# Performance work log

Measured on AMD Instinct MI355X. Metric: run time of the kernel, lower is better.

Reference implementation:

```python
import jax, jax.numpy as jnp
import numpy as np

B, L, H, S = 64, 1024, 768, 32
NH, HD = 8, H // 8
SEP = 102
EPS_LN = 1e-5


def setup_inputs() -> dict:
    key = jax.random.key(0)
    ks = jax.random.split(key, 16)
    # input_ids with exactly S SEP tokens per row at positions (j+1)*(L//S)-1
    ids = jax.random.randint(ks[0], (B, L), 1000, 30000, dtype=jnp.int64)
    sep_idx = (jnp.arange(1, S + 1) * (L // S)) - 1  # [S]
    ids = ids.at[:, sep_idx].set(SEP)
    attention_mask = jnp.ones((B, L), dtype=jnp.int32)
    labels = jax.random.randint(ks[1], (B, S), 0, 2, dtype=jnp.int64)
    sequence_output = jax.random.normal(ks[2], (B, L, H), dtype=jnp.float32)
    sc = 0.02
    params = dict(
        enc_W=jax.random.normal(ks[3], (H, H), jnp.float32) * sc,
        enc_b=jnp.zeros((H,), jnp.float32),
        enc_ln_g=jnp.ones((H,), jnp.float32),
        enc_ln_b=jnp.zeros((H,), jnp.float32),
        in_proj_W=jax.random.normal(ks[4], (3 * H, H), jnp.float32) * sc,
        in_proj_b=jnp.zeros((3 * H,), jnp.float32),
        out_proj_W=jax.random.normal(ks[5], (H, H), jnp.float32) * sc,
        out_proj_b=jnp.zeros((H,), jnp.float32),
        cls_W1=jax.random.normal(ks[6], (H, H), jnp.float32) * sc,
        cls_b1=jnp.zeros((H,), jnp.float32),
        cls_ln_g=jnp.ones((H,), jnp.float32),
        cls_ln_b=jnp.zeros((H,), jnp.float32),
        cls_W2=jax.random.normal(ks[7], (2, H), jnp.float32) * sc,
        cls_b2=jnp.zeros((2,), jnp.float32),
    )
    return dict(input_ids=ids, attention_mask=attention_mask, labels=labels,
                sequence_output=sequence_output, **params)


def _layernorm(x, g, b):
    m = jnp.mean(x, axis=-1, keepdims=True)
    v = jnp.mean((x - m) ** 2, axis=-1, keepdims=True)
    return (x - m) * jax.lax.rsqrt(v + EPS_LN) * g + b


def _gelu(x):
    return jax.nn.gelu(x, approximate=False)


def reference(input_ids, attention_mask, labels, sequence_output,
              enc_W, enc_b, enc_ln_g, enc_ln_b,
              in_proj_W, in_proj_b, out_proj_W, out_proj_b,
              cls_W1, cls_b1, cls_ln_g, cls_ln_b, cls_W2, cls_b2):
    # sep positions per sample (exactly S per row by construction)
    sep_pos = jax.vmap(lambda r: jnp.nonzero(r == SEP, size=S, fill_value=L - 1)[0])(input_ids)  # [B,S]
    all_pos = jnp.concatenate([jnp.zeros((B, 1), sep_pos.dtype), sep_pos], axis=1)  # [B,S+1]
    starts, ends = all_pos[:, :S], all_pos[:, 1:]  # inclusive [start, end] as in slice start:end+1
    t = jnp.arange(L)
    seg = (t[None, None, :] >= starts[:, :, None]) & (t[None, None, :] <= ends[:, :, None])  # [B,S,L]
    m = seg.astype(jnp.float32) * attention_mask[:, None, :].astype(jnp.float32)
    denom = jnp.sum(m, axis=-1, keepdims=True) + 1e-10  # [B,S,1]
    reps = jnp.einsum('bsl,bld->bsd', m, sequence_output) / denom  # segment mean pool
    # sentence encoder: Linear -> LN -> (dropout off) -> GELU
    x = _gelu(_layernorm(reps @ enc_W.T + enc_b, enc_ln_g, enc_ln_b))  # [B,S,H]
    # per-sample MHA (self-attention over sentences), dropout off
    qkv = x @ in_proj_W.T + in_proj_b  # [B,S,3H]
    q, k, v = jnp.split(qkv, 3, axis=-1)
    def heads(z):
        return z.reshape(B, S, NH, HD).transpose(0, 2, 1, 3)  # [B,NH,S,HD]
    q, k, v = heads(q), heads(k), heads(v)
    scores = jnp.einsum('bhqd,bhkd->bhqk', q, k) / jnp.sqrt(jnp.float32(HD))
    attn = jax.nn.softmax(scores, axis=-1)
    o = jnp.einsum('bhqk,bhkd->bhqd', attn, v).transpose(0, 2, 1, 3).reshape(B, S, H)
    attended = o @ out_proj_W.T + out_proj_b
    # classifier
    h = _gelu(_layernorm(attended @ cls_W1.T + cls_b1, cls_ln_g, cls_ln_b))
    logits = h @ cls_W2.T + cls_b2  # [B,S,2] (current_sentences == max_sentences, no padding)
    # cross entropy with ignore_index=-100
    flat_logits = logits.reshape(-1, 2)
    flat_labels = labels.reshape(-1)
    valid = flat_labels != -100
    safe = jnp.where(valid, flat_labels, 0)
    logp = jax.nn.log_softmax(flat_logits, axis=-1)
    nll = -jnp.take_along_axis(logp, safe[:, None], axis=-1)[:, 0]
    loss = jnp.sum(jnp.where(valid, nll, 0.0)) / jnp.maximum(jnp.sum(valid), 1)
    return loss, logits
```

## Files before the change

kernel.cpp:

```cpp
#include <hip/hip_runtime.h>
#include <math.h>

#define Bdim 64
#define Ldim 1024
#define Hdim 768
#define Sdim 32
#define NHdim 8
#define HDdim 96
#define SEP_ID 102

typedef unsigned short ushort_t;
typedef __attribute__((ext_vector_type(8))) short bf16x8;
typedef __attribute__((ext_vector_type(4))) float f32x4;

__device__ __forceinline__ ushort_t f2b(float f) {
    unsigned u = __builtin_bit_cast(unsigned, f);
    u += 0x7fffu + ((u >> 16) & 1u);
    return (ushort_t)(u >> 16);
}
__device__ __forceinline__ float b2f(ushort_t v) {
    unsigned u = ((unsigned)v) << 16;
    return __builtin_bit_cast(float, u);
}

__global__ __launch_bounds__(192) void prep_pool_kernel(const float* __restrict__ seq,
                                                        const int* __restrict__ ids,
                                                        const int* __restrict__ amask,
                                                        const float* __restrict__ w0,
                                                        const float* __restrict__ w1,
                                                        const float* __restrict__ w2,
                                                        const float* __restrict__ w3,
                                                        ushort_t* __restrict__ wdst,
                                                        ushort_t* __restrict__ reps) {
    int blk = blockIdx.x;
    int t = threadIdx.x;
    if (blk >= 2048) {
        int idx = (blk - 2048) * 192 + t;
        const float* src; int off;
        if (idx < 147456)      { src = w0; off = idx; }
        else if (idx < 589824) { src = w1; off = idx - 147456; }
        else if (idx < 737280) { src = w2; off = idx - 589824; }
        else                   { src = w3; off = idx - 737280; }
        float4 v = ((const float4*)src)[off];
        ushort4 ov; ov.x = f2b(v.x); ov.y = f2b(v.y); ov.z = f2b(v.z); ov.w = f2b(v.w);
        ((ushort4*)wdst)[idx] = ov;
        return;
    }
    int b = blk >> 5, s = blk & 31;
    __shared__ unsigned long long masks[18];
    const int* idrow = ids + (size_t)b * Ldim;
    int wv = t >> 6, ln = t & 63;
#pragma unroll
    for (int r = 0; r < 6; ++r) {
        int p = r * 192 + t;
        bool is = (p < Ldim) && (idrow[p] == SEP_ID);
        unsigned long long m = __ballot(is);
        if (ln == 0) masks[r * 3 + wv] = m;
    }
    __syncthreads();
    int start, end;
    {
        int need0 = s - 1, need1 = s;
        int p0 = Ldim - 1, p1 = Ldim - 1;
        int cnt = 0;
#pragma unroll
        for (int i = 0; i < 18; ++i) {
            unsigned long long mk = masks[i];
            int pc = __popcll(mk);
            int base = (i / 3) * 192 + (i % 3) * 64;
            if (need0 >= cnt && need0 < cnt + pc) {
                unsigned long long mm = mk;
                for (int j = cnt; j < need0; ++j) mm &= mm - 1;
                p0 = base + __ffsll(mm) - 1;
            }
            if (need1 >= cnt && need1 < cnt + pc) {
                unsigned long long mm = mk;
                for (int j = cnt; j < need1; ++j) mm &= mm - 1;
                p1 = base + __ffsll(mm) - 1;
            }
            cnt += pc;
        }
        start = (s == 0) ? 0 : p0;
        end = p1;
    }
    const float* base = seq + (size_t)b * Ldim * Hdim;
    const int* am = amask + b * Ldim;
    float4 A0 = {0,0,0,0}, A1 = {0,0,0,0};
    float d0 = 0.f, d1 = 0.f;
    int l = start;
    for (; l + 7 <= end; l += 8) {
        float m[8]; float4 v[8];
#pragma unroll
        for (int r = 0; r < 8; ++r) m[r] = (float)am[l + r];
#pragma unroll
        for (int r = 0; r < 8; ++r) v[r] = ((const float4*)(base + (size_t)(l + r) * Hdim))[t];
#pragma unroll
        for (int r = 0; r < 8; ++r) {
            if (r & 1) {
                d1 += m[r];
                A1.x += m[r] * v[r].x; A1.y += m[r] * v[r].y;
                A1.z += m[r] * v[r].z; A1.w += m[r] * v[r].w;
            } else {
                d0 += m[r];
                A0.x += m[r] * v[r].x; A0.y += m[r] * v[r].y;
                A0.z += m[r] * v[r].z; A0.w += m[r] * v[r].w;
            }
        }
    }
    for (; l <= end; ++l) {
        float m0 = (float)am[l];
        float4 v0 = ((const float4*)(base + (size_t)l * Hdim))[t];
        d0 += m0;
        A0.x += m0 * v0.x; A0.y += m0 * v0.y; A0.z += m0 * v0.z; A0.w += m0 * v0.w;
    }
    float denom = d0 + d1;
    float inv = 1.f / (denom + 1e-10f);
    float4 acc;
    acc.x = (A0.x + A1.x) * inv;
    acc.y = (A0.y + A1.y) * inv;
    acc.z = (A0.z + A1.z) * inv;
    acc.w = (A0.w + A1.w) * inv;
    ushort4 o;
    o.x = f2b(acc.x); o.y = f2b(acc.y); o.z = f2b(acc.z); o.w = f2b(acc.w);
    ((ushort4*)(reps + (size_t)blk * Hdim))[t] = o;
}

__global__ __launch_bounds__(256) void gemm_mfma(const ushort_t* __restrict__ A,
                                                 const ushort_t* __restrict__ W,
                                                 const float* __restrict__ bias,
                                                 ushort_t* __restrict__ Cout,
                                                 int M, int N, int K) {
    __shared__ __attribute__((aligned(16))) ushort_t Al[2][64][64];
    __shared__ __attribute__((aligned(16))) ushort_t Bl[2][64][64];
    int tid = threadIdx.x;
    int wid = tid >> 6, lane = tid & 63;
    int rowBase = blockIdx.x * 64, colBase = blockIdx.y * 64;
    int wm = (wid >> 1) * 32, wn = (wid & 1) * 32;

    int srow = lane >> 3;
    int sblk = (lane & 7) ^ srow;
    const ushort_t* Abase = A + (size_t)(rowBase + wid * 16 + srow) * K + sblk * 8;
    const ushort_t* Wbase = W + (size_t)(colBase + wid * 16 + srow) * K + sblk * 8;

    f32x4 acc[2][2] = {};

#define STAGE(bufi, kofs)                                                                    \
    do {                                                                                     \
        const ushort_t* ag = Abase + (kofs);                                                 \
        const ushort_t* wg = Wbase + (kofs);                                                 \
        __builtin_amdgcn_global_load_lds(ag,           &Al[bufi][wid * 16][0],     16, 0, 0); \
        __builtin_amdgcn_global_load_lds(ag + 8 * K,   &Al[bufi][wid * 16 + 8][0], 16, 0, 0); \
        __builtin_amdgcn_global_load_lds(wg,           &Bl[bufi][wid * 16][0],     16, 0, 0); \
        __builtin_amdgcn_global_load_lds(wg + 8 * K,   &Bl[bufi][wid * 16 + 8][0], 16, 0, 0); \
    } while (0)

    STAGE(0, 0);
    __syncthreads();
    int nk = K >> 6;
    int lr = lane & 15;
    int lxor = lane & 7;
    for (int t = 0; t < nk; ++t) {
        if (t + 1 < nk) STAGE((t + 1) & 1, (t + 1) * 64);
        int cb = t & 1;
#pragma unroll
        for (int ks = 0; ks < 2; ++ks) {
            int pblk = ((ks * 4 + (lane >> 4)) ^ lxor) * 8;
            bf16x8 af[2], wf[2];
            af[0] = *(const bf16x8*)&Al[cb][wm + lr][pblk];
            af[1] = *(const bf16x8*)&Al[cb][wm + 16 + lr][pblk];
            wf[0] = *(const bf16x8*)&Bl[cb][wn + lr][pblk];
            wf[1] = *(const bf16x8*)&Bl[cb][wn + 16 + lr][pblk];
#pragma unroll
            for (int i = 0; i < 2; ++i)
#pragma unroll
                for (int j = 0; j < 2; ++j)
                    acc[i][j] = __builtin_amdgcn_mfma_f32_16x16x32_bf16(af[i], wf[j], acc[i][j], 0, 0, 0);
        }
        __syncthreads();
    }
#undef STAGE

    int lrow = (lane >> 4) * 4, lcol = lane & 15;
#pragma unroll
    for (int ni = 0; ni < 2; ++ni) {
        int c = colBase + wn + ni * 16 + lcol;
        float bv = bias[c];
#pragma unroll
        for (int mi = 0; mi < 2; ++mi) {
            int rb = rowBase + wm + mi * 16 + lrow;
#pragma unroll
            for (int j = 0; j < 4; ++j)
                Cout[(size_t)(rb + j) * N + c] = f2b(acc[mi][ni][j] + bv);
        }
    }
}

__global__ __launch_bounds__(192) void ln_gelu(const ushort_t* __restrict__ X,
                                               const float* __restrict__ g,
                                               const float* __restrict__ bt,
                                               ushort_t* __restrict__ Y) {
    int row = blockIdx.x;
    int t = threadIdx.x;
    ushort4 v = ((const ushort4*)(X + (size_t)row * Hdim))[t];
    float vals[4] = { b2f(v.x), b2f(v.y), b2f(v.z), b2f(v.w) };
    float s = vals[0] + vals[1] + vals[2] + vals[3];
    float s2 = vals[0]*vals[0] + vals[1]*vals[1] + vals[2]*vals[2] + vals[3]*vals[3];
#pragma unroll
    for (int off = 32; off; off >>= 1) { s += __shfl_down(s, off); s2 += __shfl_down(s2, off); }
    __shared__ float red[6];
    int wid = t >> 6;
    if ((t & 63) == 0) { red[wid * 2] = s; red[wid * 2 + 1] = s2; }
    __syncthreads();
    s  = red[0] + red[2] + red[4];
    s2 = red[1] + red[3] + red[5];
    float mean = s / Hdim;
    float var  = s2 / Hdim - mean * mean;
    float rstd = rsqrtf(var + 1e-5f);
    float4 gv = ((const float4*)g)[t];
    float4 bv = ((const float4*)bt)[t];
    float gg[4] = { gv.x, gv.y, gv.z, gv.w };
    float bb[4] = { bv.x, bv.y, bv.z, bv.w };
    ushort4 o;
    ushort_t* op = (ushort_t*)&o;
#pragma unroll
    for (int i = 0; i < 4; ++i) {
        float xn = (vals[i] - mean) * rstd * gg[i] + bb[i];
        float ge = 0.5f * xn * (1.f + erff(xn * 0.70710678118654752f));
        op[i] = f2b(ge);
    }
    ((ushort4*)(Y + (size_t)row * Hdim))[t] = o;
}

__global__ __launch_bounds__(256) void attn_kernel(const ushort_t* __restrict__ qkv,
                                                   ushort_t* __restrict__ o) {
    int bh = blockIdx.x;
    int b = bh >> 3, h = bh & 7;
    __shared__ float qs[Sdim][100], ks_[Sdim][100], vs[Sdim][100];
    __shared__ float sc[Sdim][33];
    int tid = threadIdx.x;
    for (int idx = tid; idx < 2304; idx += 256) {
        int m = idx / 768;
        int w = idx - m * 768;
        int s = w / 24, d4 = (w - s * 24) * 4;
        ushort4 v = *(const ushort4*)(qkv + (size_t)(b * Sdim + s) * (3 * Hdim) + m * Hdim + h * HDdim + d4);
        float* dst = (m == 0 ? &qs[s][d4] : (m == 1 ? &ks_[s][d4] : &vs[s][d4]));
        dst[0] = b2f(v.x); dst[1] = b2f(v.y); dst[2] = b2f(v.z); dst[3] = b2f(v.w);
    }
    __syncthreads();
    int ti = tid >> 4, tj = tid & 15;
    float a00 = 0.f, a01 = 0.f, a10 = 0.f, a11 = 0.f;
#pragma unroll 6
    for (int d = 0; d < HDdim; d += 4) {
        float4 q0 = *(const float4*)&qs[ti][d];
        float4 q1 = *(const float4*)&qs[ti + 16][d];
        float4 k0 = *(const float4*)&ks_[tj][d];
        float4 k1 = *(const float4*)&ks_[tj + 16][d];
        a00 += q0.x*k0.x + q0.y*k0.y + q0.z*k0.z + q0.w*k0.w;
        a01 += q0.x*k1.x + q0.y*k1.y + q0.z*k1.z + q0.w*k1.w;
        a10 += q1.x*k0.x + q1.y*k0.y + q1.z*k0.z + q1.w*k0.w;
        a11 += q1.x*k1.x + q1.y*k1.y + q1.z*k1.z + q1.w*k1.w;
    }
    const float sscale = 0.102062072615966f;
    sc[ti][tj]           = a00 * sscale;
    sc[ti][tj + 16]      = a01 * sscale;
    sc[ti + 16][tj]      = a10 * sscale;
    sc[ti + 16][tj + 16] = a11 * sscale;
    __syncthreads();
    int row = tid >> 3, jg = tid & 7;
    float v0 = sc[row][jg], v1 = sc[row][jg + 8], v2 = sc[row][jg + 16], v3 = sc[row][jg + 24];
    float mx = fmaxf(fmaxf(v0, v1), fmaxf(v2, v3));
#pragma unroll
    for (int m = 1; m <= 4; m <<= 1) mx = fmaxf(mx, __shfl_xor(mx, m));
    v0 = expf(v0 - mx); v1 = expf(v1 - mx); v2 = expf(v2 - mx); v3 = expf(v3 - mx);
    float sum = v0 + v1 + v2 + v3;
#pragma unroll
    for (int m = 1; m <= 4; m <<= 1) sum += __shfl_xor(sum, m);
    float inv = 1.f / sum;
    sc[row][jg] = v0 * inv; sc[row][jg + 8] = v1 * inv;
    sc[row][jg + 16] = v2 * inv; sc[row][jg + 24] = v3 * inv;
    __syncthreads();
    for (int idx = tid; idx < 768; idx += 256) {
        int ii = idx / 24, d4 = (idx - ii * 24) * 4;
        float o0 = 0.f, o1 = 0.f, o2 = 0.f, o3 = 0.f;
#pragma unroll 8
        for (int j = 0; j < Sdim; ++j) {
            float p = sc[ii][j];
            float4 vv = *(const float4*)&vs[j][d4];
            o0 += p * vv.x; o1 += p * vv.y; o2 += p * vv.z; o3 += p * vv.w;
        }
        ushort4 ov; ov.x = f2b(o0); ov.y = f2b(o1); ov.z = f2b(o2); ov.w = f2b(o3);
        *(ushort4*)(o + (size_t)(b * Sdim + ii) * Hdim + h * HDdim + d4) = ov;
    }
}

__global__ __launch_bounds__(192) void cls_head_kernel(const ushort_t* __restrict__ X,
                                                       const float* __restrict__ g,
                                                       const float* __restrict__ bt,
                                                       const float* __restrict__ W2,
                                                       const float* __restrict__ b2,
                                                       float* __restrict__ out) {
    int row = blockIdx.x;
    int t = threadIdx.x;
    ushort4 v = ((const ushort4*)(X + (size_t)row * Hdim))[t];
    float vals[4] = { b2f(v.x), b2f(v.y), b2f(v.z), b2f(v.w) };
    float s = vals[0] + vals[1] + vals[2] + vals[3];
    float s2 = vals[0]*vals[0] + vals[1]*vals[1] + vals[2]*vals[2] + vals[3]*vals[3];
#pragma unroll
    for (int off = 32; off; off >>= 1) { s += __shfl_down(s, off); s2 += __shfl_down(s2, off); }
    __shared__ float red1[6], red2[6];
    int wid = t >> 6;
    if ((t & 63) == 0) { red1[wid * 2] = s; red1[wid * 2 + 1] = s2; }
    __syncthreads();
    s  = red1[0] + red1[2] + red1[4];
    s2 = red1[1] + red1[3] + red1[5];
    float mean = s / Hdim;
    float var  = s2 / Hdim - mean * mean;
    float rstd = rsqrtf(var + 1e-5f);
    float4 gv = ((const float4*)g)[t];
    float4 bv = ((const float4*)bt)[t];
    float4 w0 = ((const float4*)W2)[t];
    float4 w1 = ((const float4*)(W2 + Hdim))[t];
    float gg[4] = { gv.x, gv.y, gv.z, gv.w };
    float bb[4] = { bv.x, bv.y, bv.z, bv.w };
    float ww0[4] = { w0.x, w0.y, w0.z, w0.w };
    float ww1[4] = { w1.x, w1.y, w1.z, w1.w };
    float a0 = 0.f, a1 = 0.f;
#pragma unroll
    for (int i = 0; i < 4; ++i) {
        float xn = (vals[i] - mean) * rstd * gg[i] + bb[i];
        float ge = 0.5f * xn * (1.f + erff(xn * 0.70710678118654752f));
        a0 += ge * ww0[i];
        a1 += ge * ww1[i];
    }
#pragma unroll
    for (int off = 32; off; off >>= 1) { a0 += __shfl_down(a0, off); a1 += __shfl_down(a1, off); }
    if ((t & 63) == 0) { red2[wid * 2] = a0; red2[wid * 2 + 1] = a1; }
    __syncthreads();
    if (t == 0) {
        out[row * 2 + 0] = red2[0] + red2[2] + red2[4] + b2[0];
        out[row * 2 + 1] = red2[1] + red2[3] + red2[5] + b2[1];
    }
}

__global__ __launch_bounds__(256) void loss_kernel(const float* __restrict__ logits,
                                                   const int* __restrict__ labels,
                                                   float* __restrict__ out) {
    int t = threadIdx.x;
    float sum = 0.f, cnt = 0.f;
    for (int i = t; i < Bdim * Sdim; i += 256) {
        int lab = labels[i];
        if (lab != -100) {
            float l0 = logits[i * 2], l1 = logits[i * 2 + 1];
            float mx = fmaxf(l0, l1);
            float lse = mx + logf(expf(l0 - mx) + expf(l1 - mx));
            sum += lse - (lab ? l1 : l0);
            cnt += 1.f;
        }
    }
#pragma unroll
    for (int off = 32; off; off >>= 1) { sum += __shfl_down(sum, off); cnt += __shfl_down(cnt, off); }
    __shared__ float red[8];
    int wid = t >> 6;
    if ((t & 63) == 0) { red[wid * 2] = sum; red[wid * 2 + 1] = cnt; }
    __syncthreads();
    if (t == 0) {
        float ts = red[0] + red[2] + red[4] + red[6];
        float tc = red[1] + red[3] + red[5] + red[7];
        out[0] = ts / fmaxf(tc, 1.f);
    }
}

extern "C" void kernel_launch(void* const* d_in, const int* in_sizes, int n_in,
                              void* d_out, int out_size, void* d_ws, size_t ws_size,
                              hipStream_t stream) {
    const int*   input_ids  = (const int*)d_in[0];
    const int*   amask      = (const int*)d_in[1];
    const int*   labels     = (const int*)d_in[2];
    const float* seq        = (const float*)d_in[3];
    const float* enc_W      = (const float*)d_in[4];
    const float* enc_b      = (const float*)d_in[5];
    const float* enc_ln_g   = (const float*)d_in[6];
    const float* enc_ln_b   = (const float*)d_in[7];
    const float* in_proj_W  = (const float*)d_in[8];
    const float* in_proj_b  = (const float*)d_in[9];
    const float* out_proj_W = (const float*)d_in[10];
    const float* out_proj_b = (const float*)d_in[11];
    const float* cls_W1     = (const float*)d_in[12];
    const float* cls_b1     = (const float*)d_in[13];
    const float* cls_ln_g   = (const float*)d_in[14];
    const float* cls_ln_b   = (const float*)d_in[15];
    const float* cls_W2     = (const float*)d_in[16];
    const float* cls_b2     = (const float*)d_in[17];

    float* out = (float*)d_out;

    char* ws = (char*)d_ws;
    const size_t MS = (size_t)Bdim * Sdim;
    ushort_t* wbf     = (ushort_t*)(ws);
    ushort_t* bf_a    = (ushort_t*)(ws + 7077888);
    ushort_t* bf_b    = bf_a + MS * Hdim;
    ushort_t* bf_c    = bf_b + MS * Hdim;
    ushort_t* bf_d    = bf_c + MS * Hdim;
    ushort_t* bf_qkv  = bf_d + MS * Hdim;

    ushort_t* encWb     = wbf;
    ushort_t* inprojWb  = wbf + 589824;
    ushort_t* outprojWb = wbf + 2359296;
    ushort_t* clsW1b    = wbf + 2949120;

    prep_pool_kernel<<<6656, 192, 0, stream>>>(seq, input_ids, amask,
                                               enc_W, in_proj_W, out_proj_W, cls_W1,
                                               wbf, bf_a);
    { dim3 g(32, 12); gemm_mfma<<<g, 256, 0, stream>>>(bf_a, encWb, enc_b, bf_d, (int)MS, Hdim, Hdim); }
    ln_gelu<<<Bdim * Sdim, 192, 0, stream>>>(bf_d, enc_ln_g, enc_ln_b, bf_b);
    { dim3 g(32, 36); gemm_mfma<<<g, 256, 0, stream>>>(bf_b, inprojWb, in_proj_b, bf_qkv, (int)MS, 3 * Hdim, Hdim); }
    attn_kernel<<<Bdim * NHdim, 256, 0, stream>>>(bf_qkv, bf_c);
    { dim3 g(32, 12); gemm_mfma<<<g, 256, 0, stream>>>(bf_c, outprojWb, out_proj_b, bf_a, (int)MS, Hdim, Hdim); }
    { dim3 g(32, 12); gemm_mfma<<<g, 256, 0, stream>>>(bf_a, clsW1b, cls_b1, bf_d, (int)MS, Hdim, Hdim); }
    cls_head_kernel<<<Bdim * Sdim, 192, 0, stream>>>(bf_d, cls_ln_g, cls_ln_b, cls_W2, cls_b2, out + 1);
    loss_kernel<<<1, 256, 0, stream>>>(out + 1, labels, out);
}
```

Baseline: 116.5 us.

## Fold out_proj and cls_W1 into one combined weight and fuse loss into head

Precomputes a combined weight Wc = cls_W1 · out_proj_W and a combined bias (cls_W1·out_proj_b + cls_b1), so the two back-to-back linear layers become a single GEMM. The transpose and the weight product are computed in the prep and encoder GEMM launches, alongside existing work. The separate loss kernel is removed: the classifier head accumulates the loss with atomics and the last block writes the mean. This removes one full GEMM over the activations and one launch. It adds per-call weight-product work, rounds the fused weight to bf16 once more, and makes the loss sum order nondeterministic.

```diff
diff --git a/kernel.cpp b/kernel.cpp
--- a/kernel.cpp
+++ b/kernel.cpp
@@ -23,31 +23,90 @@
     return __builtin_bit_cast(float, u);
 }
 
-__global__ __launch_bounds__(192) void prep_pool_kernel(const float* __restrict__ seq,
-                                                        const int* __restrict__ ids,
-                                                        const int* __restrict__ amask,
-                                                        const float* __restrict__ w0,
-                                                        const float* __restrict__ w1,
-                                                        const float* __restrict__ w2,
-                                                        const float* __restrict__ w3,
-                                                        ushort_t* __restrict__ wdst,
-                                                        ushort_t* __restrict__ reps) {
+#define PREP_POOL_END   2048
+#define PREP_WC_END     5888
+#define PREP_TR_END     6032
+#define PREP_BC_END     6044
+#define PREP_TOTAL      6045
+
+__global__ __launch_bounds__(192) void prep_kernel(const float* __restrict__ seq,
+                                                   const int* __restrict__ ids,
+                                                   const int* __restrict__ amask,
+                                                   const float* __restrict__ enc_W,
+                                                   const float* __restrict__ in_proj_W,
+                                                   const float* __restrict__ cls_W1,
+                                                   const float* __restrict__ out_proj_W,
+                                                   const float* __restrict__ out_proj_b,
+                                                   const float* __restrict__ cls_b1,
+                                                   ushort_t* __restrict__ wbf,
+                                                   ushort_t* __restrict__ W3T,
+                                                   float* __restrict__ bc,
+                                                   float* __restrict__ accum,
+                                                   ushort_t* __restrict__ reps) {
+    __shared__ __attribute__((aligned(16))) char sh[8448];
     int blk = blockIdx.x;
     int t = threadIdx.x;
-    if (blk >= 2048) {
-        int idx = (blk - 2048) * 192 + t;
+
+    if (blk >= PREP_POOL_END && blk < PREP_WC_END) {
+        int idx = (blk - PREP_POOL_END) * 192 + t;
         const float* src; int off;
-        if (idx < 147456)      { src = w0; off = idx; }
-        else if (idx < 589824) { src = w1; off = idx - 147456; }
-        else if (idx < 737280) { src = w2; off = idx - 589824; }
-        else                   { src = w3; off = idx - 737280; }
+        if (idx < 147456)      { src = enc_W;     off = idx; }
+        else if (idx < 589824) { src = in_proj_W; off = idx - 147456; }
+        else                   { src = cls_W1;    off = idx - 589824; }
         float4 v = ((const float4*)src)[off];
         ushort4 ov; ov.x = f2b(v.x); ov.y = f2b(v.y); ov.z = f2b(v.z); ov.w = f2b(v.w);
-        ((ushort4*)wdst)[idx] = ov;
+        ((ushort4*)wbf)[idx] = ov;
         return;
     }
+    if (blk >= PREP_WC_END && blk < PREP_TR_END) {
+        int tile = blk - PREP_WC_END;
+        int tr = tile / 12, tc = tile % 12;
+        typedef ushort_t lds_row[65];
+        lds_row* lds = (lds_row*)sh;
+        for (int idx = t; idx < 1024; idx += 192) {
+            int r = idx >> 4, c4 = (idx & 15) << 2;
+            float4 v = *(const float4*)(out_proj_W + (size_t)(tr * 64 + r) * Hdim + tc * 64 + c4);
+            lds[c4][r]     = f2b(v.x);
+            lds[c4 + 1][r] = f2b(v.y);
+            lds[c4 + 2][r] = f2b(v.z);
+            lds[c4 + 3][r] = f2b(v.w);
+        }
+        __syncthreads();
+        for (int idx = t; idx < 1024; idx += 192) {
+            int c = idx >> 4, r4 = (idx & 15) << 2;
+            ushort4 ov;
+            ov.x = lds[c][r4]; ov.y = lds[c][r4 + 1];
+            ov.z = lds[c][r4 + 2]; ov.w = lds[c][r4 + 3];
+            *(ushort4*)(W3T + (size_t)(tc * 64 + c) * Hdim + tr * 64 + r4) = ov;
+        }
+        return;
+    }
+    if (blk >= PREP_TR_END && blk < PREP_BC_END) {
+        int bb = blk - PREP_TR_END;
+        int rl = t / 3, part = t - rl * 3;
+        int row = bb * 64 + rl;
+        const float4* wrow = (const float4*)(cls_W1 + (size_t)row * Hdim) + part * 64;
+        const float4* b3v  = (const float4*)out_proj_b + part * 64;
+        float s = 0.f;
+#pragma unroll 8
+        for (int i = 0; i < 64; ++i) {
+            float4 a = wrow[i], b = b3v[i];
+            s += a.x * b.x + a.y * b.y + a.z * b.z + a.w * b.w;
+        }
+        typedef float part_row[3];
+        part_row* pp = (part_row*)sh;
+        pp[rl][part] = s;
+        __syncthreads();
+        if (part == 0) bc[row] = pp[rl][0] + pp[rl][1] + pp[rl][2] + cls_b1[row];
+        return;
+    }
+    if (blk >= PREP_BC_END) {
+        if (t < 4) accum[t] = 0.f;
+        return;
+    }
+
     int b = blk >> 5, s = blk & 31;
-    __shared__ unsigned long long masks[18];
+    unsigned long long* masks = (unsigned long long*)sh;
     const int* idrow = ids + (size_t)b * Ldim;
     int wv = t >> 6, ln = t & 63;
 #pragma unroll
@@ -125,16 +184,16 @@
     ((ushort4*)(reps + (size_t)blk * Hdim))[t] = o;
 }
 
-__global__ __launch_bounds__(256) void gemm_mfma(const ushort_t* __restrict__ A,
-                                                 const ushort_t* __restrict__ W,
-                                                 const float* __restrict__ bias,
-                                                 ushort_t* __restrict__ Cout,
-                                                 int M, int N, int K) {
+__device__ __forceinline__ void gemm_body(const ushort_t* __restrict__ A,
+                                          const ushort_t* __restrict__ W,
+                                          const float* __restrict__ bias,
+                                          ushort_t* __restrict__ Cout,
+                                          int N, int K, int bx, int by) {
     __shared__ __attribute__((aligned(16))) ushort_t Al[2][64][64];
     __shared__ __attribute__((aligned(16))) ushort_t Bl[2][64][64];
     int tid = threadIdx.x;
     int wid = tid >> 6, lane = tid & 63;
-    int rowBase = blockIdx.x * 64, colBase = blockIdx.y * 64;
+    int rowBase = bx * 64, colBase = by * 64;
     int wm = (wid >> 1) * 32, wn = (wid & 1) * 32;
 
     int srow = lane >> 3;
@@ -184,7 +243,7 @@
 #pragma unroll
     for (int ni = 0; ni < 2; ++ni) {
         int c = colBase + wn + ni * 16 + lcol;
-        float bv = bias[c];
+        float bv = bias ? bias[c] : 0.f;
 #pragma unroll
         for (int mi = 0; mi < 2; ++mi) {
             int rb = rowBase + wm + mi * 16 + lrow;
@@ -193,6 +252,30 @@
                 Cout[(size_t)(rb + j) * N + c] = f2b(acc[mi][ni][j] + bv);
         }
     }
+}
+
+__global__ __launch_bounds__(256) void gemm_enc_wc(const ushort_t* __restrict__ reps,
+                                                   const ushort_t* __restrict__ encWb,
+                                                   const float* __restrict__ enc_b,
+                                                   ushort_t* __restrict__ outD,
+                                                   const ushort_t* __restrict__ W4b,
+                                                   const ushort_t* __restrict__ W3Tb,
+                                                   ushort_t* __restrict__ Wcb) {
+    int blk = blockIdx.x;
+    if (blk < 384) {
+        gemm_body(reps, encWb, enc_b, outD, Hdim, Hdim, blk & 31, blk >> 5);
+    } else {
+        int t2 = blk - 384;
+        gemm_body(W4b, W3Tb, (const float*)nullptr, Wcb, Hdim, Hdim, t2 % 12, t2 / 12);
+    }
+}
+
+__global__ __launch_bounds__(256) void gemm_mfma(const ushort_t* __restrict__ A,
+                                                 const ushort_t* __restrict__ W,
+                                                 const float* __restrict__ bias,
+                                                 ushort_t* __restrict__ Cout,
+                                                 int N, int K) {
+    gemm_body(A, W, bias, Cout, N, K, blockIdx.x, blockIdx.y);
 }
 
 __global__ __launch_bounds__(192) void ln_gelu(const ushort_t* __restrict__ X,
@@ -293,12 +376,14 @@
     }
 }
 
-__global__ __launch_bounds__(192) void cls_head_kernel(const ushort_t* __restrict__ X,
-                                                       const float* __restrict__ g,
-                                                       const float* __restrict__ bt,
-                                                       const float* __restrict__ W2,
-                                                       const float* __restrict__ b2,
-                                                       float* __restrict__ out) {
+__global__ __launch_bounds__(192) void cls_head_loss(const ushort_t* __restrict__ X,
+                                                     const float* __restrict__ g,
+                                                     const float* __restrict__ bt,
+                                                     const float* __restrict__ W2,
+                                                     const float* __restrict__ b2,
+                                                     const int* __restrict__ labels,
+                                                     float* __restrict__ accum,
+                                                     float* __restrict__ out) {
     int row = blockIdx.x;
     int t = threadIdx.x;
     ushort4 v = ((const ushort4*)(X + (size_t)row * Hdim))[t];
@@ -337,36 +422,24 @@
     if ((t & 63) == 0) { red2[wid * 2] = a0; red2[wid * 2 + 1] = a1; }
     __syncthreads();
     if (t == 0) {
-        out[row * 2 + 0] = red2[0] + red2[2] + red2[4] + b2[0];
-        out[row * 2 + 1] = red2[1] + red2[3] + red2[5] + b2[1];
-    }
-}
-
-__global__ __launch_bounds__(256) void loss_kernel(const float* __restrict__ logits,
-                                                   const int* __restrict__ labels,
-                                                   float* __restrict__ out) {
-    int t = threadIdx.x;
-    float sum = 0.f, cnt = 0.f;
-    for (int i = t; i < Bdim * Sdim; i += 256) {
-        int lab = labels[i];
+        float l0 = red2[0] + red2[2] + red2[4] + b2[0];
+        float l1 = red2[1] + red2[3] + red2[5] + b2[1];
+        out[1 + row * 2]     = l0;
+        out[1 + row * 2 + 1] = l1;
+        int lab = labels[row];
         if (lab != -100) {
-            float l0 = logits[i * 2], l1 = logits[i * 2 + 1];
             float mx = fmaxf(l0, l1);
             float lse = mx + logf(expf(l0 - mx) + expf(l1 - mx));
-            sum += lse - (lab ? l1 : l0);
-            cnt += 1.f;
-        }
-    }
-#pragma unroll
-    for (int off = 32; off; off >>= 1) { sum += __shfl_down(sum, off); cnt += __shfl_down(cnt, off); }
-    __shared__ float red[8];
-    int wid = t >> 6;
-    if ((t & 63) == 0) { red[wid * 2] = sum; red[wid * 2 + 1] = cnt; }
-    __syncthreads();
-    if (t == 0) {
-        float ts = red[0] + red[2] + red[4] + red[6];
-        float tc = red[1] + red[3] + red[5] + red[7];
-        out[0] = ts / fmaxf(tc, 1.f);
+            atomicAdd(&accum[0], lse - (lab ? l1 : l0));
+            atomicAdd(&accum[1], 1.0f);
+        }
+        __threadfence();
+        int old = atomicAdd((int*)&accum[2], 1);
+        if (old == Bdim * Sdim - 1) {
+            float ts = atomicAdd(&accum[0], 0.0f);
+            float tc = atomicAdd(&accum[1], 0.0f);
+            out[0] = ts / fmaxf(tc, 1.f);
+        }
     }
 }
 
@@ -396,27 +469,29 @@
 
     char* ws = (char*)d_ws;
     const size_t MS = (size_t)Bdim * Sdim;
-    ushort_t* wbf     = (ushort_t*)(ws);
-    ushort_t* bf_a    = (ushort_t*)(ws + 7077888);
-    ushort_t* bf_b    = bf_a + MS * Hdim;
-    ushort_t* bf_c    = bf_b + MS * Hdim;
-    ushort_t* bf_d    = bf_c + MS * Hdim;
-    ushort_t* bf_qkv  = bf_d + MS * Hdim;
-
-    ushort_t* encWb     = wbf;
-    ushort_t* inprojWb  = wbf + 589824;
-    ushort_t* outprojWb = wbf + 2359296;
-    ushort_t* clsW1b    = wbf + 2949120;
-
-    prep_pool_kernel<<<6656, 192, 0, stream>>>(seq, input_ids, amask,
-                                               enc_W, in_proj_W, out_proj_W, cls_W1,
-                                               wbf, bf_a);
-    { dim3 g(32, 12); gemm_mfma<<<g, 256, 0, stream>>>(bf_a, encWb, enc_b, bf_d, (int)MS, Hdim, Hdim); }
+    ushort_t* wbf   = (ushort_t*)ws;
+    ushort_t* encWb    = wbf;
+    ushort_t* inprojWb = wbf + 589824;
+    ushort_t* W4b      = wbf + 2359296;
+    ushort_t* W3Tb     = wbf + 2949120;
+    ushort_t* Wcb      = wbf + 3538944;
+    float*    bc    = (float*)(ws + 8257536);
+    float*    accum = (float*)(ws + 8260608);
+    ushort_t* bf_a  = (ushort_t*)(ws + 8260672);
+    ushort_t* bf_b  = bf_a + MS * Hdim;
+    ushort_t* bf_c  = bf_b + MS * Hdim;
+    ushort_t* bf_d  = bf_c + MS * Hdim;
+    ushort_t* bf_qkv = bf_d + MS * Hdim;
+
+    prep_kernel<<<PREP_TOTAL, 192, 0, stream>>>(seq, input_ids, amask,
+                                                enc_W, in_proj_W, cls_W1,
+                                                out_proj_W, out_proj_b, cls_b1,
+                                                wbf, W3Tb, bc, accum, bf_a);
+    gemm_enc_wc<<<528, 256, 0, stream>>>(bf_a, encWb, enc_b, bf_d, W4b, W3Tb, Wcb);
     ln_gelu<<<Bdim * Sdim, 192, 0, stream>>>(bf_d, enc_ln_g, enc_ln_b, bf_b);
-    { dim3 g(32, 36); gemm_mfma<<<g, 256, 0, stream>>>(bf_b, inprojWb, in_proj_b, bf_qkv, (int)MS, 3 * Hdim, Hdim); }
+    { dim3 g(32, 36); gemm_mfma<<<g, 256, 0, stream>>>(bf_b, inprojWb, in_proj_b, bf_qkv, 3 * Hdim, Hdim); }
     attn_kernel<<<Bdim * NHdim, 256, 0, stream>>>(bf_qkv, bf_c);
-    { dim3 g(32, 12); gemm_mfma<<<g, 256, 0, stream>>>(bf_c, outprojWb, out_proj_b, bf_a, (int)MS, Hdim, Hdim); }
-    { dim3 g(32, 12); gemm_mfma<<<g, 256, 0, stream>>>(bf_a, clsW1b, cls_b1, bf_d, (int)MS, Hdim, Hdim); }
-    cls_head_kernel<<<Bdim * Sdim, 192, 0, stream>>>(bf_d, cls_ln_g, cls_ln_b, cls_W2, cls_b2, out + 1);
-    loss_kernel<<<1, 256, 0, stream>>>(out + 1, labels, out);
-}
+    { dim3 g(32, 12); gemm_mfma<<<g, 256, 0, stream>>>(bf_c, Wcb, bc, bf_d, Hdim, Hdim); }
+    cls_head_loss<<<Bdim * Sdim, 192, 0, stream>>>(bf_d, cls_ln_g, cls_ln_b,
+                                                   cls_W2, cls_b2, labels, accum, out);
+}
```

New measurement: 197.0 us. +69.1%, slower.
